# Kernel tuning notes

Hardware: AMD Instinct MI355X
Metric: run time of the kernel (lower is better)

## Reference

```python
import jax, jax.numpy as jnp
import numpy as np

D = 512       # input_embedding_dimensions
H = 2         # num_heads
HD = D // H   # head_dim = 256
B = 16
S = 1194      # max_sequence_length


def setup_inputs() -> dict:
    key = jax.random.key(0)
    k1, k2, k3, k4, k5 = jax.random.split(key, 5)
    scale_in = 1.0 / np.sqrt(D)
    return {
        "positional_embeddings": jax.random.normal(k1, (B, S, D), dtype=jnp.float32),
        "W_qkv": jax.random.uniform(k2, (D, 3 * D), minval=-scale_in, maxval=scale_in, dtype=jnp.float32),
        "b_qkv": jax.random.uniform(k3, (3 * D,), minval=-scale_in, maxval=scale_in, dtype=jnp.float32),
        "W_out": jax.random.uniform(k4, (D, D), minval=-scale_in, maxval=scale_in, dtype=jnp.float32),
        "b_out": jax.random.uniform(k5, (D,), minval=-scale_in, maxval=scale_in, dtype=jnp.float32),
    }


def reference(positional_embeddings, W_qkv, b_qkv, W_out, b_out):
    x = positional_embeddings              # [B, S, D]
    b, s, _ = x.shape
    qkv = x @ W_qkv + b_qkv                # [B, S, 3D]
    q, k, v = jnp.split(qkv, 3, axis=-1)

    def split_heads(t):
        return t.reshape(b, s, H, HD).transpose(0, 2, 1, 3)  # [B, H, S, HD]

    q, k, v = split_heads(q), split_heads(k), split_heads(v)
    scores = jnp.einsum("bhqd,bhkd->bhqk", q, k) / jnp.sqrt(jnp.float32(HD))
    causal = jnp.tril(jnp.ones((s, s), dtype=bool))          # [S, S]
    scores = jnp.where(causal[None, None, :, :], scores, -jnp.inf)
    att = jax.nn.softmax(scores, axis=-1)                    # [B, H, S, S]
    out = jnp.einsum("bhqk,bhkd->bhqd", att, v)              # [B, H, S, HD]
    out = out.transpose(0, 2, 1, 3).reshape(b, s, D)         # [B, S, D]
    return out @ W_out + b_out
```

## Files before the change

### kernel.cpp

```cpp
#include <hip/hip_runtime.h>
#include <stdint.h>

#define D_    512
#define H_    2
#define HD_   256
#define B_    16
#define S_    1194
#define MTOK  19104
#define MPAD  19200
#define SPAD  1216
#define NQKV  1536
#define NKT   38
#define LOG2E 1.44269504088896340736f

typedef unsigned short u16;
typedef __attribute__((ext_vector_type(8))) short bf16x8;
typedef __attribute__((ext_vector_type(4))) float f32x4;

__device__ inline u16 f2bf(float x) {
  union { float f; unsigned u; } c; c.f = x;
  unsigned r = c.u + 0x7fffu + ((c.u >> 16) & 1u);
  return (u16)(r >> 16);
}

__device__ inline void async_copy16(void* lds, const void* g) {
  __builtin_amdgcn_global_load_lds(
      (__attribute__((address_space(1))) void*)(g),
      (__attribute__((address_space(3))) void*)(lds),
      16, 0, 0);
}

__global__ void convert_kernel(const float* __restrict__ X,
                               const float* __restrict__ Wqkv,
                               const float* __restrict__ Wout,
                               u16* __restrict__ Xf,
                               u16* __restrict__ Wqf,
                               u16* __restrict__ Wof) {
  const int NXG = MPAD * 64;
  const int NQG = 12 * 8 * 16 * 64;
  const int NOG = 4 * 8 * 16 * 64;
  const int TOT = NXG + NQG + NOG;
  int stride = gridDim.x * blockDim.x;
  for (int g = blockIdx.x * blockDim.x + threadIdx.x; g < TOT; g += stride) {
    if (g < NXG) {
      int lane = g & 63, f = (g >> 6) & 15, kt = (g >> 10) & 7, mt = g >> 13;
      int i = mt * 128 + (f & 7) * 16 + (lane & 15);
      int k = kt * 64 + (f >> 3) * 32 + (lane >> 4) * 8;
      bf16x8 o;
      if (i < MTOK) {
        f32x4 v0 = *(const f32x4*)&X[(size_t)i * 512 + k];
        f32x4 v1 = *(const f32x4*)&X[(size_t)i * 512 + k + 4];
#pragma unroll
        for (int e = 0; e < 4; ++e) { o[e] = (short)f2bf(v0[e]); o[4 + e] = (short)f2bf(v1[e]); }
      } else {
#pragma unroll
        for (int e = 0; e < 8; ++e) o[e] = 0;
      }
      *(bf16x8*)&Xf[(size_t)g * 8] = o;
    } else if (g < NXG + NQG) {
      int gg = g - NXG;
      int lane = gg & 63, f = (gg >> 6) & 15, kt = (gg >> 10) & 7, nt = gg >> 13;
      int j = nt * 128 + (f & 7) * 16 + (lane & 15);
      int k = kt * 64 + (f >> 3) * 32 + (lane >> 4) * 8;
      bf16x8 o;
#pragma unroll
      for (int e = 0; e < 8; ++e) o[e] = (short)f2bf(Wqkv[(size_t)(k + e) * NQKV + j]);
      *(bf16x8*)&Wqf[(size_t)gg * 8] = o;
    } else {
      int gg = g - NXG - NQG;
      int lane = gg & 63, f = (gg >> 6) & 15, kt = (gg >> 10) & 7, nt = gg >> 13;
      int j = nt * 128 + (f & 7) * 16 + (lane & 15);
      int k = kt * 64 + (f >> 3) * 32 + (lane >> 4) * 8;
      bf16x8 o;
#pragma unroll
      for (int e = 0; e < 8; ++e) o[e] = (short)f2bf(Wout[(size_t)(k + e) * 512 + j]);
      *(bf16x8*)&Wof[(size_t)gg * 8] = o;
    }
  }
}

template<int MODE>
__global__ __launch_bounds__(256, 2) void gemm_kernel(
    const u16* __restrict__ Af, const u16* __restrict__ Bf,
    const float* __restrict__ bias, int nb,
    u16* __restrict__ Qb, u16* __restrict__ Kf, u16* __restrict__ Vf,
    float* __restrict__ Cout)
{
  __shared__ u16 ldsA[16 * 512];
  __shared__ u16 ldsB[16 * 512];

  const int t  = threadIdx.x;
  const int l  = t & 63;
  const int w  = t >> 6;
  const int lr = l >> 4, lc = l & 15;

  const int nwg = gridDim.x;
  const int qq = nwg >> 3, rr8 = nwg & 7;
  const int xcd = blockIdx.x & 7, off = blockIdx.x >> 3;
  const int wgid = (xcd < rr8 ? xcd * (qq + 1) : rr8 * (qq + 1) + (xcd - rr8) * qq) + off;
  const int m0 = (wgid / nb) * 128;
  const int n0 = (wgid % nb) * 128;

  const u16* pA = Af + ((size_t)(m0 >> 7) * 128 + w) * 512 + l * 8;
  const u16* pB = Bf + ((size_t)(n0 >> 7) * 128 + w) * 512 + l * 8;

  f32x4 acc[4][4] = {};

  for (int kt = 0; kt < 8; ++kt) {
    __syncthreads();
    const u16* qA = pA + kt * 8192;
    const u16* qB = pB + kt * 8192;
#pragma unroll
    for (int c = 0; c < 4; ++c) {
      async_copy16(&ldsA[(c * 4 + w) * 512], qA + c * 2048);
      async_copy16(&ldsB[(c * 4 + w) * 512], qB + c * 2048);
    }
    __syncthreads();
#pragma unroll
    for (int kk = 0; kk < 2; ++kk) {
      bf16x8 af[4], bfr[4];
#pragma unroll
      for (int m = 0; m < 4; ++m)
        af[m] = *(bf16x8*)&ldsA[((kk * 8 + (w >> 1) * 4 + m) * 64 + l) * 8];
#pragma unroll
      for (int n = 0; n < 4; ++n)
        bfr[n] = *(bf16x8*)&ldsB[((kk * 8 + (w & 1) * 4 + n) * 64 + l) * 8];
      __builtin_amdgcn_s_setprio(1);
#pragma unroll
      for (int m = 0; m < 4; ++m)
#pragma unroll
        for (int n = 0; n < 4; ++n)
          acc[m][n] = __builtin_amdgcn_mfma_f32_16x16x32_bf16(af[m], bfr[n], acc[m][n], 0, 0, 0);
      __builtin_amdgcn_s_setprio(0);
    }
  }

  int jv[4]; float bj[4];
#pragma unroll
  for (int n = 0; n < 4; ++n) { jv[n] = n0 + (w & 1) * 64 + n * 16 + lc; bj[n] = bias[jv[n]]; }

#pragma unroll
  for (int m = 0; m < 4; ++m) {
#pragma unroll
    for (int r = 0; r < 4; ++r) {
      int i = m0 + (w >> 1) * 64 + m * 16 + lr * 4 + r;
      if (i >= MTOK) continue;
      if (MODE == 0) {
        int b = i / S_, s = i - b * S_;
        int stK  = s >> 5;
        int nfs  = (s >> 4) & 1;
        int lisK = s & 15;
        int lvhi = (s >> 3) & 3;
        int es   = s & 7;
#pragma unroll
        for (int n = 0; n < 4; ++n) {
          int j = jv[n];
          int which = j >> 9, h = (j >> 8) & 1, d = j & 255;
          int bh = b * H_ + h;
          u16 v = f2bf(acc[m][n][r] + bj[n]);
          if (which == 0) {
            Qb[((size_t)(bh * SPAD + s)) * HD_ + d] = v;
          } else if (which == 1) {
            Kf[(((size_t)(bh * NKT + stK)) * 16 + (d >> 5) * 2 + nfs) * 512 +
               (((d >> 3) & 3) * 16 + lisK) * 8 + (d & 7)] = v;
          } else {
            Vf[(((size_t)(bh * NKT + stK)) * 16 + (d >> 4)) * 512 +
               (lvhi * 16 + (d & 15)) * 8 + es] = v;
          }
        }
      } else {
#pragma unroll
        for (int n = 0; n < 4; ++n)
          Cout[(size_t)i * D_ + jv[n]] = acc[m][n][r] + bj[n];
      }
    }
  }
}

__global__ __launch_bounds__(256, 2) void attn_kernel(
    const u16* __restrict__ Qb, const u16* __restrict__ Kf,
    const u16* __restrict__ Vf, u16* __restrict__ Obf)
{
  __shared__ u16 ldsP[4][16 * 36];

  const int id   = blockIdx.x;
  const int xcd  = id & 7;
  const int slot = id >> 3;
  const int bh   = xcd + 8 * (slot / 19);
  const int qt   = 18 - (slot % 19);
  const int q0   = qt * 64;
  const int nkv  = 2 * qt + 2;
  const int t  = threadIdx.x, l = t & 63, w = t >> 6;
  const int lr = l >> 4, lc = l & 15;
  const int wq0 = q0 + w * 16;
  const int qrow_l = wq0 + lc;

  bf16x8 qf[8];
  const u16* qbase = Qb + (size_t)(bh * SPAD + qrow_l) * HD_ + lr * 8;
#pragma unroll
  for (int kb = 0; kb < 8; ++kb)
    qf[kb] = *(const bf16x8*)(qbase + kb * 32);

  f32x4 oacc[16] = {};
  float mrow = -1e30f, lsum = 0.f;

  const u16* kroot = Kf + (((size_t)(bh * NKT)) * 16) * 512 + l * 8;
  const u16* vroot = Vf + (((size_t)(bh * NKT)) * 16) * 512 + l * 8;

  for (int kt = 0; kt < nkv; ++kt) {
    bf16x8 kv[16];
    {
      const u16* kb_ = kroot + (size_t)kt * 16 * 512;
#pragma unroll
      for (int f = 0; f < 16; ++f)
        kv[f] = *(const bf16x8*)(kb_ + f * 512);
    }

    f32x4 sacc[2] = {};
    __builtin_amdgcn_s_setprio(1);
#pragma unroll
    for (int kb = 0; kb < 8; ++kb) {
#pragma unroll
      for (int nf = 0; nf < 2; ++nf)
        sacc[nf] = __builtin_amdgcn_mfma_f32_16x16x32_bf16(kv[kb * 2 + nf], qf[kb], sacc[nf], 0, 0, 0);
    }
    __builtin_amdgcn_s_setprio(0);

    {
      const u16* vb_ = vroot + (size_t)kt * 16 * 512;
#pragma unroll
      for (int f = 0; f < 16; ++f)
        kv[f] = *(const bf16x8*)(vb_ + f * 512);
    }

    const int kv0 = kt * 32;
    float sv[2][4];
    float pm = -1e30f;
    if (kv0 + 31 <= wq0) {
#pragma unroll
      for (int nf = 0; nf < 2; ++nf)
#pragma unroll
        for (int r = 0; r < 4; ++r) {
          float v = sacc[nf][r] * 0.0625f;
          sv[nf][r] = v;
          pm = fmaxf(pm, v);
        }
    } else {
#pragma unroll
      for (int nf = 0; nf < 2; ++nf)
#pragma unroll
        for (int r = 0; r < 4; ++r) {
          int kvi = kv0 + nf * 16 + lr * 4 + r;
          float v = ((kvi <= qrow_l) && (kvi < S_)) ? sacc[nf][r] * 0.0625f : -1e30f;
          sv[nf][r] = v;
          pm = fmaxf(pm, v);
        }
    }
    pm = fmaxf(pm, __shfl_xor(pm, 16));
    pm = fmaxf(pm, __shfl_xor(pm, 32));

    bool skip = (pm <= mrow + 8.0f);
    if (!__all(skip)) {
      float mn = fmaxf(mrow, pm);
      float sc = exp2f((mrow - mn) * LOG2E);
      mrow = mn;
      lsum *= sc;
#pragma unroll
      for (int nf = 0; nf < 16; ++nf)
#pragma unroll
        for (int r = 0; r < 4; ++r) oacc[nf][r] *= sc;
    }

#pragma unroll
    for (int nf = 0; nf < 2; ++nf) {
      float p0 = exp2f((sv[nf][0] - mrow) * LOG2E);
      float p1 = exp2f((sv[nf][1] - mrow) * LOG2E);
      float p2 = exp2f((sv[nf][2] - mrow) * LOG2E);
      float p3 = exp2f((sv[nf][3] - mrow) * LOG2E);
      lsum += (p0 + p1) + (p2 + p3);
      uint64_t pk = (uint64_t)f2bf(p0) | ((uint64_t)f2bf(p1) << 16) |
                    ((uint64_t)f2bf(p2) << 32) | ((uint64_t)f2bf(p3) << 48);
      *(uint64_t*)&ldsP[w][lc * 36 + nf * 16 + lr * 4] = pk;
    }

    bf16x8 pf = *(bf16x8*)&ldsP[w][lc * 36 + lr * 8];
    __builtin_amdgcn_s_setprio(1);
#pragma unroll
    for (int nf = 0; nf < 16; ++nf)
      oacc[nf] = __builtin_amdgcn_mfma_f32_16x16x32_bf16(kv[nf], pf, oacc[nf], 0, 0, 0);
    __builtin_amdgcn_s_setprio(0);
  }

  float s = lsum;
  s += __shfl_xor(s, 16);
  s += __shfl_xor(s, 32);
  float inv = 1.0f / s;

  const int b = bh >> 1, h = bh & 1;
  if (qrow_l < S_) {
    int i = b * S_ + qrow_l;
    int it = i >> 7, mf = (i >> 4) & 7, li = i & 15;
#pragma unroll
    for (int nf = 0; nf < 16; ++nf) {
#pragma unroll
      for (int r = 0; r < 4; ++r) {
        int j = h * HD_ + nf * 16 + lr * 4 + r;
        size_t addr = (((size_t)(it * 8 + (j >> 6))) * 16 + ((j >> 5) & 1) * 8 + mf) * 512 +
                      (((j >> 3) & 3) * 16 + li) * 8 + (j & 7);
        Obf[addr] = f2bf(oacc[nf][r] * inv);
      }
    }
  }
}

extern "C" void kernel_launch(void* const* d_in, const int* in_sizes, int n_in,
                              void* d_out, int out_size, void* d_ws, size_t ws_size,
                              hipStream_t stream) {
  const float* X    = (const float*)d_in[0];
  const float* Wqkv = (const float*)d_in[1];
  const float* bqkv = (const float*)d_in[2];
  const float* Wout = (const float*)d_in[3];
  const float* bout = (const float*)d_in[4];
  float* out = (float*)d_out;

  char* ws = (char*)d_ws;
  u16* Xf  = (u16*)ws;  ws += (size_t)MPAD * D_ * 2;
  u16* Wqf = (u16*)ws;  ws += (size_t)NQKV * D_ * 2;
  u16* Wof = (u16*)ws;  ws += (size_t)D_ * D_ * 2;
  u16* Qb  = (u16*)ws;  ws += (size_t)B_ * H_ * SPAD * HD_ * 2;
  u16* Kf  = (u16*)ws;  ws += (size_t)B_ * H_ * SPAD * HD_ * 2;
  u16* Vf  = (u16*)ws;  ws += (size_t)B_ * H_ * SPAD * HD_ * 2;
  u16* Obf = (u16*)ws;  ws += (size_t)MPAD * D_ * 2;

  convert_kernel<<<2048, 256, 0, stream>>>(X, Wqkv, Wout, Xf, Wqf, Wof);
  gemm_kernel<0><<<1800, 256, 0, stream>>>(Xf, Wqf, bqkv, 12, Qb, Kf, Vf, nullptr);
  attn_kernel<<<608, 256, 0, stream>>>(Qb, Kf, Vf, Obf);
  gemm_kernel<1><<<600, 256, 0, stream>>>(Obf, Wof, bout, 4, nullptr, nullptr, nullptr, out);
}
```

Before: 159.8 us.

## Share K tiles via double-buffered LDS async copies and software-pipeline QK^T

K tiles are now loaded once per block into a double-buffered LDS buffer with async copies, so the four waves no longer each fetch the same K fragments from global memory. The score MFMA for the next tile is issued before the PV MFMA of the current tile, overlapping softmax with tensor work. This adds block-wide barriers each iteration and 32KB of LDS, which may lower occupancy. It depends on an async_copy16 helper defined elsewhere.

Result: faster. 152.1 us (-4.9%).

```diff
diff --git a/kernel.cpp b/kernel.cpp
--- a/kernel.cpp
+++ b/kernel.cpp
@@ -181,6 +181,7 @@
     const u16* __restrict__ Qb, const u16* __restrict__ Kf,
     const u16* __restrict__ Vf, u16* __restrict__ Obf)
 {
+  __shared__ u16 ldsK[2][16 * 512];
   __shared__ u16 ldsP[4][16 * 36];
 
   const int id   = blockIdx.x;
@@ -204,92 +205,122 @@
   f32x4 oacc[16] = {};
   float mrow = -1e30f, lsum = 0.f;
 
-  const u16* kroot = Kf + (((size_t)(bh * NKT)) * 16) * 512 + l * 8;
-  const u16* vroot = Vf + (((size_t)(bh * NKT)) * 16) * 512 + l * 8;
-
-  for (int kt = 0; kt < nkv; ++kt) {
-    bf16x8 kv[16];
-    {
-      const u16* kb_ = kroot + (size_t)kt * 16 * 512;
-#pragma unroll
-      for (int f = 0; f < 16; ++f)
-        kv[f] = *(const bf16x8*)(kb_ + f * 512);
-    }
-
-    f32x4 sacc[2] = {};
-    __builtin_amdgcn_s_setprio(1);
-#pragma unroll
-    for (int kb = 0; kb < 8; ++kb) {
-#pragma unroll
-      for (int nf = 0; nf < 2; ++nf)
-        sacc[nf] = __builtin_amdgcn_mfma_f32_16x16x32_bf16(kv[kb * 2 + nf], qf[kb], sacc[nf], 0, 0, 0);
-    }
-    __builtin_amdgcn_s_setprio(0);
-
-    {
-      const u16* vb_ = vroot + (size_t)kt * 16 * 512;
-#pragma unroll
-      for (int f = 0; f < 16; ++f)
-        kv[f] = *(const bf16x8*)(vb_ + f * 512);
-    }
-
-    const int kv0 = kt * 32;
-    float sv[2][4];
-    float pm = -1e30f;
-    if (kv0 + 31 <= wq0) {
-#pragma unroll
-      for (int nf = 0; nf < 2; ++nf)
-#pragma unroll
-        for (int r = 0; r < 4; ++r) {
-          float v = sacc[nf][r] * 0.0625f;
-          sv[nf][r] = v;
-          pm = fmaxf(pm, v);
-        }
-    } else {
-#pragma unroll
-      for (int nf = 0; nf < 2; ++nf)
-#pragma unroll
-        for (int r = 0; r < 4; ++r) {
-          int kvi = kv0 + nf * 16 + lr * 4 + r;
-          float v = ((kvi <= qrow_l) && (kvi < S_)) ? sacc[nf][r] * 0.0625f : -1e30f;
-          sv[nf][r] = v;
-          pm = fmaxf(pm, v);
-        }
-    }
-    pm = fmaxf(pm, __shfl_xor(pm, 16));
-    pm = fmaxf(pm, __shfl_xor(pm, 32));
-
-    bool skip = (pm <= mrow + 8.0f);
-    if (!__all(skip)) {
-      float mn = fmaxf(mrow, pm);
-      float sc = exp2f((mrow - mn) * LOG2E);
-      mrow = mn;
-      lsum *= sc;
-#pragma unroll
-      for (int nf = 0; nf < 16; ++nf)
-#pragma unroll
-        for (int r = 0; r < 4; ++r) oacc[nf][r] *= sc;
-    }
-
+  const u16* kroot = Kf + ((size_t)(bh * NKT) * 16 + w) * 512 + l * 8;
+  const u16* vroot = Vf + ((size_t)(bh * NKT) * 16) * 512 + l * 8;
+
+#pragma unroll
+  for (int c = 0; c < 4; ++c) {
+    async_copy16(&ldsK[0][(c * 4 + w) * 512], kroot + c * 2048);
+    async_copy16(&ldsK[1][(c * 4 + w) * 512], kroot + 8192 + c * 2048);
+  }
+  __syncthreads();
+
+  f32x4 saccA[2] = {}, saccB[2] = {};
+  __builtin_amdgcn_s_setprio(1);
+#pragma unroll
+  for (int kb = 0; kb < 8; ++kb)
 #pragma unroll
     for (int nf = 0; nf < 2; ++nf) {
-      float p0 = exp2f((sv[nf][0] - mrow) * LOG2E);
-      float p1 = exp2f((sv[nf][1] - mrow) * LOG2E);
-      float p2 = exp2f((sv[nf][2] - mrow) * LOG2E);
-      float p3 = exp2f((sv[nf][3] - mrow) * LOG2E);
-      lsum += (p0 + p1) + (p2 + p3);
-      uint64_t pk = (uint64_t)f2bf(p0) | ((uint64_t)f2bf(p1) << 16) |
-                    ((uint64_t)f2bf(p2) << 32) | ((uint64_t)f2bf(p3) << 48);
-      *(uint64_t*)&ldsP[w][lc * 36 + nf * 16 + lr * 4] = pk;
-    }
-
-    bf16x8 pf = *(bf16x8*)&ldsP[w][lc * 36 + lr * 8];
-    __builtin_amdgcn_s_setprio(1);
-#pragma unroll
-    for (int nf = 0; nf < 16; ++nf)
-      oacc[nf] = __builtin_amdgcn_mfma_f32_16x16x32_bf16(kv[nf], pf, oacc[nf], 0, 0, 0);
-    __builtin_amdgcn_s_setprio(0);
-  }
+      bf16x8 kf = *(bf16x8*)&ldsK[0][((kb * 2 + nf) * 64 + l) * 8];
+      saccA[nf] = __builtin_amdgcn_mfma_f32_16x16x32_bf16(kf, qf[kb], saccA[nf], 0, 0, 0);
+    }
+  __builtin_amdgcn_s_setprio(0);
+  __syncthreads();
+
+#define SUBITER(J, S, N)                                                       \
+  {                                                                            \
+    const int j_ = (J);                                                        \
+    bf16x8 vfr[16];                                                            \
+    {                                                                          \
+      const u16* vb_ = vroot + (size_t)j_ * 8192;                              \
+      _Pragma("unroll")                                                        \
+      for (int f = 0; f < 16; ++f) vfr[f] = *(const bf16x8*)(vb_ + f * 512);   \
+    }                                                                          \
+    if (j_ + 2 < nkv) {                                                        \
+      const u16* kb_ = kroot + (size_t)(j_ + 2) * 8192;                        \
+      _Pragma("unroll")                                                        \
+      for (int c = 0; c < 4; ++c)                                              \
+        async_copy16(&ldsK[j_ & 1][(c * 4 + w) * 512], kb_ + c * 2048);        \
+    }                                                                          \
+    const int kv0 = j_ * 32;                                                   \
+    float sv[2][4];                                                            \
+    float pm = -1e30f;                                                         \
+    if (kv0 + 31 <= wq0) {                                                     \
+      _Pragma("unroll")                                                        \
+      for (int nf = 0; nf < 2; ++nf)                                           \
+        _Pragma("unroll")                                                      \
+        for (int r = 0; r < 4; ++r) {                                          \
+          float v = S[nf][r] * 0.0625f;                                        \
+          sv[nf][r] = v;                                                       \
+          pm = fmaxf(pm, v);                                                   \
+        }                                                                      \
+    } else {                                                                   \
+      _Pragma("unroll")                                                        \
+      for (int nf = 0; nf < 2; ++nf)                                           \
+        _Pragma("unroll")                                                      \
+        for (int r = 0; r < 4; ++r) {                                          \
+          int kvi = kv0 + nf * 16 + lr * 4 + r;                                \
+          float v = ((kvi <= qrow_l) && (kvi < S_)) ? S[nf][r] * 0.0625f       \
+                                                    : -1e30f;                  \
+          sv[nf][r] = v;                                                       \
+          pm = fmaxf(pm, v);                                                   \
+        }                                                                      \
+    }                                                                          \
+    pm = fmaxf(pm, __shfl_xor(pm, 16));                                        \
+    pm = fmaxf(pm, __shfl_xor(pm, 32));                                        \
+    bool skip = (pm <= mrow + 8.0f);                                           \
+    if (!__all(skip)) {                                                        \
+      float mn = fmaxf(mrow, pm);                                              \
+      float sc = exp2f((mrow - mn) * LOG2E);                                   \
+      mrow = mn;                                                               \
+      lsum *= sc;                                                              \
+      _Pragma("unroll")                                                        \
+      for (int nf = 0; nf < 16; ++nf)                                          \
+        _Pragma("unroll")                                                      \
+        for (int r = 0; r < 4; ++r) oacc[nf][r] *= sc;                         \
+    }                                                                          \
+    _Pragma("unroll")                                                          \
+    for (int nf = 0; nf < 2; ++nf) {                                           \
+      float p0 = exp2f((sv[nf][0] - mrow) * LOG2E);                            \
+      float p1 = exp2f((sv[nf][1] - mrow) * LOG2E);                            \
+      float p2 = exp2f((sv[nf][2] - mrow) * LOG2E);                            \
+      float p3 = exp2f((sv[nf][3] - mrow) * LOG2E);                            \
+      lsum += (p0 + p1) + (p2 + p3);                                           \
+      uint64_t pk = (uint64_t)f2bf(p0) | ((uint64_t)f2bf(p1) << 16) |          \
+                    ((uint64_t)f2bf(p2) << 32) | ((uint64_t)f2bf(p3) << 48);   \
+      *(uint64_t*)&ldsP[w][lc * 36 + nf * 16 + lr * 4] = pk;                   \
+    }                                                                          \
+    if (j_ + 1 < nkv) {                                                        \
+      N[0] = (f32x4){0.f, 0.f, 0.f, 0.f};                                      \
+      N[1] = (f32x4){0.f, 0.f, 0.f, 0.f};                                      \
+      __builtin_amdgcn_s_setprio(1);                                           \
+      _Pragma("unroll")                                                        \
+      for (int kb = 0; kb < 8; ++kb)                                           \
+        _Pragma("unroll")                                                      \
+        for (int nf = 0; nf < 2; ++nf) {                                       \
+          bf16x8 kf =                                                          \
+              *(bf16x8*)&ldsK[(j_ + 1) & 1][((kb * 2 + nf) * 64 + l) * 8];     \
+          N[nf] = __builtin_amdgcn_mfma_f32_16x16x32_bf16(kf, qf[kb], N[nf],   \
+                                                          0, 0, 0);            \
+        }                                                                      \
+      __builtin_amdgcn_s_setprio(0);                                           \
+    }                                                                          \
+    __syncthreads();                                                           \
+    bf16x8 pf = *(bf16x8*)&ldsP[w][lc * 36 + lr * 8];                          \
+    __builtin_amdgcn_s_setprio(1);                                             \
+    _Pragma("unroll")                                                          \
+    for (int nf = 0; nf < 16; ++nf)                                            \
+      oacc[nf] =                                                               \
+          __builtin_amdgcn_mfma_f32_16x16x32_bf16(vfr[nf], pf, oacc[nf],       \
+                                                  0, 0, 0);                    \
+    __builtin_amdgcn_s_setprio(0);                                             \
+  }
+
+  for (int kt = 0; kt < nkv; kt += 2) {
+    SUBITER(kt, saccA, saccB);
+    SUBITER(kt + 1, saccB, saccA);
+  }
+#undef SUBITER
 
   float s = lsum;
   s += __shfl_xor(s, 16);
```
